# Performance work log

Hardware: AMD Instinct MI355X
Metric: run time of the kernel (lower is better)

## Reference

```python
import jax, jax.numpy as jnp
import numpy as np

B, S, DIM = 8, 4096, 512
G, V = 2, 320            # num_groups, num_vars
CVD = 256                # codevector_dim
D = CVD // G             # per-group codevector dim = 128
TAU = 2.0                # gumbel temperature


def setup_inputs() -> dict:
    key = jax.random.key(0)
    k1, k2, k3, k4 = jax.random.split(key, 4)
    hidden_states = jax.random.normal(k1, (B, S, DIM), dtype=jnp.float32)
    # weight_proj: Linear(dim -> G*V)
    W = jax.random.normal(k2, (DIM, G * V), dtype=jnp.float32) * 0.02
    b = jnp.zeros((G * V,), dtype=jnp.float32)
    # codebook: torch init is uniform(0,1) on [1, G*V, D]; store as [G*V, D]
    codevectors = jax.random.uniform(k3, (G * V, D), dtype=jnp.float32)
    # standard Gumbel(0,1) noise, one row per (token, group)
    u = jax.random.uniform(k4, (B * S * G, V), dtype=jnp.float32,
                           minval=1e-6, maxval=1.0 - 1e-6)
    gumbels = -jnp.log(-jnp.log(u))
    return {"hidden_states": hidden_states, "W": W, "b": b,
            "codevectors": codevectors, "gumbels": gumbels}


def reference(hidden_states, W, b, codevectors, gumbels):
    Bc, Sc, _ = hidden_states.shape
    T = Bc * Sc
    # weight projection -> logits over codebook entries
    logits = hidden_states @ W + b                      # [B, S, G*V]
    flat = logits.reshape(T * G, V)                     # [T*G, V]

    # gumbel_softmax(hard=True) with straight-through estimator
    y_soft = jax.nn.softmax((flat + gumbels) / TAU, axis=-1)
    hard = jax.nn.one_hot(jnp.argmax(y_soft, axis=-1), V, dtype=y_soft.dtype)
    codevector_probs = hard + y_soft - jax.lax.stop_gradient(y_soft)

    # soft distribution (no gumbel noise, no temperature) per torch code
    codevector_dist = jax.nn.softmax(flat.reshape(T, G, V), axis=-1)

    # one-hot weighted sum over codebook = per-group contraction
    cb = codevectors.reshape(G, V, D)                   # [G, V, D]
    out = jnp.einsum('tgv,gvd->tgd',
                     codevector_probs.reshape(T, G, V), cb)
    out = out.reshape(Bc, Sc, G * D)                    # [B, S, codevector_dim]
    return (out, codevector_dist)
```

## Files before the change

### kernel.cpp

```cpp
#include <hip/hip_runtime.h>

#define Tcnt 32768
#define Gn   2
#define Vn   320
#define Dn   128
#define DIMK 512
#define GV   640
#define RB   128
#define NCAND 8

typedef __attribute__((ext_vector_type(8))) short bf16x8;
typedef __attribute__((ext_vector_type(4))) ushort u16x4;
typedef __attribute__((ext_vector_type(4))) float f32x4;

__device__ inline ushort f2bf(float x) {
    unsigned u = __float_as_uint(x);
    return (ushort)((u + 0x7fffu + ((u >> 16) & 1u)) >> 16);
}

#define AS1(p) ((const __attribute__((address_space(1))) void*)(p))
#define AS3(p) ((__attribute__((address_space(3))) void*)(p))

__global__ __launch_bounds__(256) void prep_wt(
    const float* __restrict__ W, ushort* __restrict__ Wt)
{
    __shared__ ushort Ls[64][72];
    int t = blockIdx.x;
    int n0 = (t % 10) * 64, k0 = (t / 10) * 64;
    int ln = threadIdx.x & 63, kq = threadIdx.x >> 6;
    #pragma unroll
    for (int kk = 0; kk < 16; ++kk) {
        int k = kq * 16 + kk;
        Ls[k][ln] = f2bf(W[(size_t)(k0 + k) * GV + n0 + ln]);
    }
    __syncthreads();
    #pragma unroll
    for (int nn = 0; nn < 16; ++nn) {
        int n = kq * 16 + nn;
        Wt[(size_t)(n0 + n) * DIMK + k0 + ln] = Ls[ln][n];
    }
}

__global__ __launch_bounds__(1024, 4) void fused_vq_kernel(
    const float*  __restrict__ hs,
    const ushort* __restrict__ Wt,
    const float*  __restrict__ W,
    const float*  __restrict__ bias,
    const float*  __restrict__ gum,
    const float*  __restrict__ cv,
    float* __restrict__ out,
    float* __restrict__ dist)
{
    union SMem {
        struct { ushort As[2][RB * 32]; ushort Bs[2][Vn * 32]; } gm;
        struct {
            float4 part[RB][2];
            int    cnt[RB];
            int    col[RB][NCAND];
            float  sc[RB][NCAND];
            float  gmv[RB][NCAND];
            int    bidx[RB];
            float  mxs[RB];
        } ep;
    };
    __shared__ SMem U;

    const int tid = threadIdx.x, w = tid >> 6, lane = tid & 63;
    const int Q = lane >> 4, c16 = lane & 15;
    const int wm = (w >> 1) * 16, wn = (w & 1) * 160, half = w & 1;

    const int bid = blockIdx.x;
    const int swz = (bid & 7) * 64 + (bid >> 3);
    const int g = swz & 1;
    const size_t t0 = (size_t)(swz >> 1) * RB;

    const int arow_s = tid >> 3, pc = tid & 7;
    const int lq = (pc >> 1) ^ ((arow_s >> 1) & 3);
    const int lc = lq * 2 + (pc & 1);
    const float* asrc = hs + (t0 + arow_s) * DIMK + lc * 4;
    const ushort* wtg = Wt + (size_t)g * Vn * DIMK;

    auto stageB = [&](int buf, int k0) {
        {
            int s = tid;
            int n = s >> 2, pq = s & 3, lqq = pq ^ ((n >> 1) & 3);
            __builtin_amdgcn_global_load_lds(
                AS1(wtg + (size_t)n * DIMK + k0 + lqq * 8),
                AS3(&U.gm.Bs[buf][s * 8]), 16, 0, 0);
        }
        if (tid < 256) {
            int s = 1024 + tid;
            int n = s >> 2, pq = s & 3, lqq = pq ^ ((n >> 1) & 3);
            __builtin_amdgcn_global_load_lds(
                AS1(wtg + (size_t)n * DIMK + k0 + lqq * 8),
                AS3(&U.gm.Bs[buf][s * 8]), 16, 0, 0);
        }
    };
    auto writeA = [&](int buf, float4 v) {
        u16x4 o;
        o[0] = f2bf(v.x); o[1] = f2bf(v.y); o[2] = f2bf(v.z); o[3] = f2bf(v.w);
        *(u16x4*)&U.gm.As[buf][tid * 4] = o;
    };

    float4 areg0 = *(const float4*)(asrc);
    stageB(0, 0);
    float4 areg1 = *(const float4*)(asrc + 32);
    writeA(0, areg0);
    __syncthreads();

    f32x4 acc[10];
    #pragma unroll
    for (int j = 0; j < 10; ++j) acc[j] = (f32x4){0.f, 0.f, 0.f, 0.f};

    #pragma unroll
    for (int ks = 0; ks < 16; ++ks) {
        if (ks + 2 < 16) {
            if ((ks & 1) == 0) areg0 = *(const float4*)(asrc + (ks + 2) * 32);
            else               areg1 = *(const float4*)(asrc + (ks + 2) * 32);
        }
        if (ks + 1 < 16) stageB((ks + 1) & 1, (ks + 1) * 32);

        const ushort* Ab = U.gm.As[ks & 1];
        const ushort* Bb = U.gm.Bs[ks & 1];
        const int ar = wm + c16;
        bf16x8 af = *(const bf16x8*)&Ab[(ar * 4 + (Q ^ ((ar >> 1) & 3))) * 8];
        #pragma unroll
        for (int j = 0; j < 10; ++j) {
            int n = wn + j * 16 + c16;
            bf16x8 bv = *(const bf16x8*)&Bb[(n * 4 + (Q ^ ((n >> 1) & 3))) * 8];
            acc[j] = __builtin_amdgcn_mfma_f32_16x16x32_bf16(af, bv, acc[j], 0, 0, 0);
        }
        if (ks + 1 < 16) writeA((ks + 1) & 1, ((ks + 1) & 1) ? areg1 : areg0);
        __syncthreads();
    }

    #pragma unroll
    for (int j = 0; j < 10; ++j) {
        float bb = bias[g * Vn + wn + j * 16 + c16];
        acc[j][0] += bb; acc[j][1] += bb; acc[j][2] += bb; acc[j][3] += bb;
    }

    if (tid < RB) U.ep.cnt[tid] = 0;
    __syncthreads();

    const float MARGIN = 0.0625f;

    #pragma unroll
    for (int qr = 0; qr < 4; ++qr) {
        int row = wm + Q * 4 + qr;
        size_t r2 = (t0 + row) * 2 + g;
        const float* gr = gum + r2 * Vn + wn;
        float sv[10];
        float mxl = -1e30f, mxs = -1e30f; int bi = 0;
        #pragma unroll
        for (int j = 0; j < 10; ++j) {
            float lg = acc[j][qr];
            float gu = gr[j * 16 + c16];
            float s = lg + gu; sv[j] = s;
            mxl = fmaxf(mxl, lg);
            if (s > mxs) { mxs = s; bi = wn + j * 16 + c16; }
        }
        #pragma unroll
        for (int off = 1; off < 16; off <<= 1) {
            mxl = fmaxf(mxl, __shfl_xor(mxl, off));
            float os = __shfl_xor(mxs, off); int ob = __shfl_xor(bi, off);
            if (os > mxs || (os == mxs && ob < bi)) { mxs = os; bi = ob; }
        }
        float sum = 0.f;
        #pragma unroll
        for (int j = 0; j < 10; ++j) sum += __expf(acc[j][qr] - mxl);
        #pragma unroll
        for (int off = 1; off < 16; off <<= 1) sum += __shfl_xor(sum, off);

        float thr = mxs - MARGIN;
        #pragma unroll
        for (int j = 0; j < 10; ++j) {
            if (sv[j] >= thr) {
                int pos = atomicAdd(&U.ep.cnt[row], 1);
                if (pos < NCAND) {
                    U.ep.col[row][pos] = wn + j * 16 + c16;
                    U.ep.sc[row][pos]  = sv[j];
                    U.ep.gmv[row][pos] = sv[j] - acc[j][qr];
                }
            }
        }
        if (c16 == 0)
            U.ep.part[row][half] = (float4){mxl, sum, mxs, __int_as_float(bi)};
    }
    __syncthreads();

    #pragma unroll
    for (int qr = 0; qr < 4; ++qr) {
        int row = wm + Q * 4 + qr;
        size_t r2 = (t0 + row) * 2 + g;
        float4 mine = U.ep.part[row][half];
        float4 oth  = U.ep.part[row][half ^ 1];
        float mxl_f = fmaxf(mine.x, oth.x);
        float sum_f = mine.y * __expf(mine.x - mxl_f) + oth.y * __expf(oth.x - mxl_f);
        float inv = 1.0f / sum_f;
        float* dr = dist + r2 * Vn + wn;
        #pragma unroll
        for (int j = 0; j < 10; ++j)
            dr[j * 16 + c16] = __expf(acc[j][qr] - mxl_f) * inv;
        if (half == 0 && c16 == 0) {
            float ms = mine.z; int mi = __float_as_int(mine.w);
            float os = oth.z;  int oi = __float_as_int(oth.w);
            if (os > ms || (os == ms && oi < mi)) { ms = os; mi = oi; }
            U.ep.mxs[row] = ms; U.ep.bidx[row] = mi;
        }
    }
    __syncthreads();

    for (int ui = 0; ui < 8; ++ui) {
        int u = w * 8 + ui;
        int c = U.ep.cnt[u]; if (c > NCAND) c = NCAND;
        float thr = U.ep.mxs[u] - MARGIN;
        int nf = 0;
        for (int j = 0; j < c; ++j) nf += (U.ep.sc[u][j] >= thr) ? 1 : 0;
        if (nf > 1) {
            size_t t = t0 + u;
            const float* hr = hs + t * DIMK;
            float4 h0 = *(const float4*)(hr + lane * 8);
            float4 h1 = *(const float4*)(hr + lane * 8 + 4);
            float hv[8] = {h0.x, h0.y, h0.z, h0.w, h1.x, h1.y, h1.z, h1.w};
            float best = -1e30f; int bv2 = 1 << 30;
            for (int j = 0; j < c; ++j) {
                if (U.ep.sc[u][j] < thr) continue;
                int v = U.ep.col[u][j];
                int gcol = g * Vn + v;
                const float* wc = W + gcol;
                float p = 0.f;
                #pragma unroll
                for (int i = 0; i < 8; ++i)
                    p = fmaf(hv[i], wc[(size_t)(lane * 8 + i) * GV], p);
                #pragma unroll
                for (int off = 1; off < 64; off <<= 1) p += __shfl_xor(p, off);
                float se = p + bias[gcol] + U.ep.gmv[u][j];
                if (se > best || (se == best && v < bv2)) { best = se; bv2 = v; }
            }
            if (lane == 0) U.ep.bidx[u] = bv2;
        }
    }
    __syncthreads();

    for (int ui = 0; ui < 8; ++ui) {
        int u = w * 8 + ui;
        size_t t = t0 + u;
        int b = U.ep.bidx[u];
        const float2* cvr = (const float2*)(cv + ((size_t)(g * Vn + b)) * Dn);
        float2 val = cvr[lane];
        *(float2*)(out + t * (Gn * Dn) + g * Dn + lane * 2) = val;
    }
}

extern "C" void kernel_launch(void* const* d_in, const int* in_sizes, int n_in,
                              void* d_out, int out_size, void* d_ws, size_t ws_size,
                              hipStream_t stream) {
    const float* hs  = (const float*)d_in[0];
    const float* W   = (const float*)d_in[1];
    const float* b   = (const float*)d_in[2];
    const float* cv  = (const float*)d_in[3];
    const float* gum = (const float*)d_in[4];

    float* out  = (float*)d_out;
    float* dist = out + (size_t)Tcnt * (Gn * Dn);
    ushort* Wt  = (ushort*)d_ws;

    prep_wt<<<80, 256, 0, stream>>>(W, Wt);
    fused_vq_kernel<<<(Tcnt / RB) * Gn, 1024, 0, stream>>>(hs, Wt, W, b, gum, cv, out, dist);
}
```

Baseline: 92.33 us.

## Load A fragments directly into registers and halve row block size

Drops LDS staging of the activation tile. Each lane now loads its own fp32 A fragment from global memory, converts it to bf16 in registers and feeds the MFMA directly. The row block shrinks from 128 to 64 and blocks from 1024 to 512 threads, doubling grid size to raise occupancy and cut LDS traffic and writes. In exchange, each wave reads hidden states with a less coalesced pattern, and the weight tile is reloaded into LDS by twice as many blocks.

```diff
diff --git a/kernel.cpp b/kernel.cpp
--- a/kernel.cpp
+++ b/kernel.cpp
@@ -1,4 +1,5 @@
 #include <hip/hip_runtime.h>
+#include <hip/hip_bf16.h>
 
 #define Tcnt 32768
 #define Gn   2
@@ -6,16 +7,26 @@
 #define Dn   128
 #define DIMK 512
 #define GV   640
-#define RB   128
+#define RB   64
 #define NCAND 8
 
 typedef __attribute__((ext_vector_type(8))) short bf16x8;
-typedef __attribute__((ext_vector_type(4))) ushort u16x4;
+typedef __attribute__((ext_vector_type(8))) ushort u16x8;
 typedef __attribute__((ext_vector_type(4))) float f32x4;
 
 __device__ inline ushort f2bf(float x) {
     unsigned u = __float_as_uint(x);
     return (ushort)((u + 0x7fffu + ((u >> 16) & 1u)) >> 16);
+}
+__device__ inline ushort nbf(float x) {
+    __hip_bfloat16 h = __float2bfloat16(x);
+    return *reinterpret_cast<ushort*>(&h);
+}
+__device__ inline bf16x8 cvt8(float4 a, float4 b) {
+    u16x8 o;
+    o[0]=nbf(a.x); o[1]=nbf(a.y); o[2]=nbf(a.z); o[3]=nbf(a.w);
+    o[4]=nbf(b.x); o[5]=nbf(b.y); o[6]=nbf(b.z); o[7]=nbf(b.w);
+    return (bf16x8)o;
 }
 
 #define AS1(p) ((const __attribute__((address_space(1))) void*)(p))
@@ -41,7 +52,7 @@
     }
 }
 
-__global__ __launch_bounds__(1024, 4) void fused_vq_kernel(
+__global__ __launch_bounds__(512, 6) void fused_vq_kernel(
     const float*  __restrict__ hs,
     const ushort* __restrict__ Wt,
     const float*  __restrict__ W,
@@ -52,7 +63,7 @@
     float* __restrict__ dist)
 {
     union SMem {
-        struct { ushort As[2][RB * 32]; ushort Bs[2][Vn * 32]; } gm;
+        ushort Bs[2][Vn * 32];
         struct {
             float4 part[RB][2];
             int    cnt[RB];
@@ -70,42 +81,35 @@
     const int wm = (w >> 1) * 16, wn = (w & 1) * 160, half = w & 1;
 
     const int bid = blockIdx.x;
-    const int swz = (bid & 7) * 64 + (bid >> 3);
+    const int swz = (bid & 7) * 128 + (bid >> 3);
     const int g = swz & 1;
     const size_t t0 = (size_t)(swz >> 1) * RB;
 
-    const int arow_s = tid >> 3, pc = tid & 7;
-    const int lq = (pc >> 1) ^ ((arow_s >> 1) & 3);
-    const int lc = lq * 2 + (pc & 1);
-    const float* asrc = hs + (t0 + arow_s) * DIMK + lc * 4;
     const ushort* wtg = Wt + (size_t)g * Vn * DIMK;
+    const float*  abase = hs + (t0 + wm + c16) * DIMK + Q * 8;
 
     auto stageB = [&](int buf, int k0) {
-        {
-            int s = tid;
+        #pragma unroll
+        for (int i2 = 0; i2 < 2; ++i2) {
+            int s = i2 * 512 + tid;
             int n = s >> 2, pq = s & 3, lqq = pq ^ ((n >> 1) & 3);
             __builtin_amdgcn_global_load_lds(
                 AS1(wtg + (size_t)n * DIMK + k0 + lqq * 8),
-                AS3(&U.gm.Bs[buf][s * 8]), 16, 0, 0);
-        }
-        if (tid < 256) {
+                AS3(&U.Bs[buf][s * 8]), 16, 0, 0);
+        }
+        if (w < 4) {
             int s = 1024 + tid;
             int n = s >> 2, pq = s & 3, lqq = pq ^ ((n >> 1) & 3);
             __builtin_amdgcn_global_load_lds(
                 AS1(wtg + (size_t)n * DIMK + k0 + lqq * 8),
-                AS3(&U.gm.Bs[buf][s * 8]), 16, 0, 0);
+                AS3(&U.Bs[buf][s * 8]), 16, 0, 0);
         }
     };
-    auto writeA = [&](int buf, float4 v) {
-        u16x4 o;
-        o[0] = f2bf(v.x); o[1] = f2bf(v.y); o[2] = f2bf(v.z); o[3] = f2bf(v.w);
-        *(u16x4*)&U.gm.As[buf][tid * 4] = o;
-    };
-
-    float4 areg0 = *(const float4*)(asrc);
+
     stageB(0, 0);
-    float4 areg1 = *(const float4*)(asrc + 32);
-    writeA(0, areg0);
+    float4 aC0 = *(const float4*)(abase);
+    float4 aC1 = *(const float4*)(abase + 4);
+    float4 aN0, aN1;
     __syncthreads();
 
     f32x4 acc[10];
@@ -114,24 +118,21 @@
 
     #pragma unroll
     for (int ks = 0; ks < 16; ++ks) {
-        if (ks + 2 < 16) {
-            if ((ks & 1) == 0) areg0 = *(const float4*)(asrc + (ks + 2) * 32);
-            else               areg1 = *(const float4*)(asrc + (ks + 2) * 32);
-        }
-        if (ks + 1 < 16) stageB((ks + 1) & 1, (ks + 1) * 32);
-
-        const ushort* Ab = U.gm.As[ks & 1];
-        const ushort* Bb = U.gm.Bs[ks & 1];
-        const int ar = wm + c16;
-        bf16x8 af = *(const bf16x8*)&Ab[(ar * 4 + (Q ^ ((ar >> 1) & 3))) * 8];
+        if (ks < 15) {
+            stageB((ks + 1) & 1, (ks + 1) * 32);
+            aN0 = *(const float4*)(abase + (ks + 1) * 32);
+            aN1 = *(const float4*)(abase + (ks + 1) * 32 + 4);
+        }
+        bf16x8 af = cvt8(aC0, aC1);
+        const ushort* Bb = U.Bs[ks & 1];
         #pragma unroll
         for (int j = 0; j < 10; ++j) {
             int n = wn + j * 16 + c16;
             bf16x8 bv = *(const bf16x8*)&Bb[(n * 4 + (Q ^ ((n >> 1) & 3))) * 8];
             acc[j] = __builtin_amdgcn_mfma_f32_16x16x32_bf16(af, bv, acc[j], 0, 0, 0);
         }
-        if (ks + 1 < 16) writeA((ks + 1) & 1, ((ks + 1) & 1) ? areg1 : areg0);
         __syncthreads();
+        aC0 = aN0; aC1 = aN1;
     }
 
     #pragma unroll
@@ -267,5 +268,5 @@
     ushort* Wt  = (ushort*)d_ws;
 
     prep_wt<<<80, 256, 0, stream>>>(W, Wt);
-    fused_vq_kernel<<<(Tcnt / RB) * Gn, 1024, 0, stream>>>(hs, Wt, W, b, gum, cv, out, dist);
-}
+    fused_vq_kernel<<<(Tcnt / RB) * Gn, 512, 0, stream>>>(hs, Wt, W, b, gum, cv, out, dist);
+}
```

Result: slower. 180.6 us (+95.6%).
